# Performance work log

Measured on AMD Instinct MI355X. Metric: run time of the kernel, lower is better.

Reference implementation:

```python
import jax, jax.numpy as jnp
import numpy as np

IN_F = 256
LAYERS = [256, 256, 256, 256]   # layer_sizeList
DIMS = [IN_F] + LAYERS          # per-layer (in, out) = (DIMS[i], DIMS[i+1])
NUM_L = len(LAYERS)             # 4 dynamic layers (3 hidden + final identity)
CASE_IN = 64
CASE_H = 256
W_SIZE = IN_F * LAYERS[0]       # 65536, uniform across layers here
C, N = 64, 2048


def setup_inputs() -> dict:
    key = jax.random.key(0)
    k = jax.random.split(key, 8)
    x = jax.random.normal(k[0], (N, IN_F), jnp.float32)
    o = jax.random.normal(k[1], (C, CASE_IN), jnp.float32)
    # caseNN hidden layer (Linear + SiLU)
    Wc = jax.random.normal(k[2], (CASE_IN, CASE_H), jnp.float32) / np.sqrt(CASE_IN).astype(np.float32)
    bc = jnp.zeros((CASE_H,), jnp.float32)
    # final heads (identity activation): one weight head + one bias head per domain layer
    head_scale = np.float32(1.0 / (np.sqrt(CASE_H) * np.sqrt(IN_F)))
    Ww = jax.random.normal(k[3], (NUM_L, CASE_H, W_SIZE), jnp.float32) * head_scale
    bw = jnp.zeros((NUM_L, W_SIZE), jnp.float32)
    Wb = jax.random.normal(k[4], (NUM_L, CASE_H, LAYERS[0]), jnp.float32) * head_scale
    bb = jnp.zeros((NUM_L, LAYERS[0]), jnp.float32)
    return {"x": x, "o": o, "Wc": Wc, "bc": bc, "Ww": Ww, "bw": bw, "Wb": Wb, "bb": bb}


def reference(x, o, Wc, bc, Ww, bw, Wb, bb):
    # ---- caseNN (hypernetwork): generate per-case weights/biases ----
    h = jax.nn.silu(o @ Wc + bc)                     # [C, H]
    w = jnp.einsum('ch,lhd->lcd', h, Ww) + bw[:, None, :]   # [L, C, in*out]
    b = jnp.einsum('ch,lhd->lcd', h, Wb) + bb[:, None, :]   # [L, C, out]
    c = o.shape[0]

    # ---- domain net: per-case dynamic FC layers with skip connections ----
    # layer 0: broadcast shared x over cases
    W0 = w[0].reshape(c, DIMS[0], DIMS[1])
    y = jax.nn.silu(jnp.einsum('ni,cio->cno', x, W0) + b[0][:, None, :])  # [C, N, 256]
    x_skip = y  # skip_connections and i==0
    for i in range(1, NUM_L - 1):
        Wi = w[i].reshape(c, DIMS[i], DIMS[i + 1])
        y2 = jax.nn.silu(jnp.einsum('cni,cio->cno', y, Wi) + b[i][:, None, :])
        if i % 2 == 0:
            y2, x_skip = y2 + x_skip, y2
        y = y2
    # final layer: identity activation
    Wf = w[NUM_L - 1].reshape(c, DIMS[NUM_L - 1], DIMS[NUM_L])
    out = jnp.einsum('cni,cio->cno', y, Wf) + b[NUM_L - 1][:, None, :]
    return out.reshape(-1, out.shape[-1])  # [C*N, out]
```

## Files before the change

### kernel.cpp

```cpp
#include <hip/hip_runtime.h>


typedef __bf16 bf16;
typedef __bf16 bf16x4 __attribute__((ext_vector_type(4)));
typedef __bf16 bf16x8 __attribute__((ext_vector_type(8)));
typedef float  f32x2  __attribute__((ext_vector_type(2)));
typedef float  f32x4  __attribute__((ext_vector_type(4)));
typedef unsigned short u16x8 __attribute__((ext_vector_type(8)));

#define AS1 __attribute__((address_space(1)))
#define AS3 __attribute__((address_space(3)))

__device__ __forceinline__ void gl2lds16(const void* g, void* l) {
  __builtin_amdgcn_global_load_lds((const AS1 unsigned int*)g,
                                   (AS3 unsigned int*)l, 16, 0, 0);
}

__device__ __forceinline__ float silu_f(float v) {
  return v / (1.0f + __expf(-v));
}

__global__ void k_hyper(const float* __restrict__ o, const float* __restrict__ Wc,
                        const float* __restrict__ bc, float* __restrict__ ht) {
  __shared__ float os[64];
  int c = blockIdx.x;
  int j = threadIdx.x;
  if (j < 64) os[j] = o[c * 64 + j];
  __syncthreads();
  float a = bc[j];
#pragma unroll
  for (int i = 0; i < 64; ++i) a = fmaf(os[i], Wc[i * 256 + j], a);
  ht[j * 64 + c] = silu_f(a);
}

__global__ void k_xcast(const float* __restrict__ x, bf16* __restrict__ xb) {
  int i = (blockIdx.x * 256 + threadIdx.x) * 4;
  float4 v = *(const float4*)(x + i);
  bf16x4 r = { (bf16)v.x, (bf16)v.y, (bf16)v.z, (bf16)v.w };
  *(bf16x4*)(xb + i) = r;
}

__global__ __launch_bounds__(256, 4) void k_genw(const float* __restrict__ Ww,
                                                 const float* __restrict__ bw,
                                                 const float* __restrict__ ht,
                                                 bf16* __restrict__ wnat) {
  int l = blockIdx.x >> 8;
  int d = (blockIdx.x & 255) * 256 + threadIdx.x;
  const float* wp = Ww + (size_t)l * 256 * 65536 + d;
  f32x2 acc[32];
#pragma unroll
  for (int c = 0; c < 32; ++c) acc[c] = (f32x2){0.f, 0.f};
  float wcur = wp[0];
  for (int hh = 0; hh < 256; ++hh) {
    float wnext = (hh < 255) ? wp[(size_t)(hh + 1) * 65536] : 0.f;
    const f32x2* hp = (const f32x2*)(ht + hh * 64);
    f32x2 wv = {wcur, wcur};
#pragma unroll
    for (int c = 0; c < 32; ++c) {
      f32x2 h2 = hp[c];
      acc[c].x = fmaf(h2.x, wv.x, acc[c].x);
      acc[c].y = fmaf(h2.y, wv.y, acc[c].y);
    }
    wcur = wnext;
  }
  float bv = bw[(size_t)l * 65536 + d];
#pragma unroll
  for (int c = 0; c < 32; ++c) {
    wnat[(size_t)(l * 64 + 2 * c) * 65536 + d]     = (bf16)(acc[c].x + bv);
    wnat[(size_t)(l * 64 + 2 * c + 1) * 65536 + d] = (bf16)(acc[c].y + bv);
  }
}

__global__ void k_genb(const float* __restrict__ Wb, const float* __restrict__ bb,
                       const float* __restrict__ ht, float* __restrict__ bias) {
  int l = blockIdx.x >> 6;
  int c = blockIdx.x & 63;
  int oo = threadIdx.x;
  const float* wp = Wb + (size_t)l * 65536 + oo;
  float acc = 0.f;
  for (int hh = 0; hh < 256; ++hh)
    acc = fmaf(ht[hh * 64 + c], wp[hh * 256], acc);
  bias[(size_t)(l * 64 + c) * 256 + oo] = acc + bb[l * 256 + oo];
}

__global__ void k_tw(const unsigned short* __restrict__ w,
                     unsigned short* __restrict__ wt) {
  __shared__ unsigned short T[64][64];
  int b = blockIdx.x;
  int lc = b >> 4, tile = b & 15;
  int i0 = (tile >> 2) << 6, o0 = (tile & 3) << 6;
  const unsigned short* src = w + (size_t)lc * 65536;
  unsigned short* dst = wt + (size_t)lc * 65536;
  int t = threadIdx.x;
  for (int q = t; q < 512; q += 256) {
    int r = q >> 3, cc = q & 7;
    u16x8 v = *(const u16x8*)(src + (size_t)(i0 + r) * 256 + o0 + cc * 8);
    *(u16x8*)&T[r][(cc ^ ((r >> 3) & 7)) * 8] = v;
  }
  __syncthreads();
  for (int q = t; q < 512; q += 256) {
    int r = q >> 3, cc = q & 7;
    u16x8 v;
#pragma unroll
    for (int e = 0; e < 8; ++e) {
      int il = cc * 8 + e;
      v[e] = T[il][((((r >> 3) ^ (il >> 3)) & 7) << 3) + (r & 7)];
    }
    *(u16x8*)(dst + (size_t)(o0 + r) * 256 + i0 + cc * 8) = v;
  }
}

template <int LAYER>
__global__ __launch_bounds__(256, 3) void k_gemm(
    const bf16* __restrict__ A_base, const bf16* __restrict__ WT,
    const float* __restrict__ BIAS, bf16* __restrict__ Yout,
    const bf16* __restrict__ Skip, float* __restrict__ Fout) {
  __shared__ bf16 As[128 * 32];
  __shared__ bf16 Bs[128 * 32];
  int bx = blockIdx.x;
  bx = (bx & 7) * 256 + (bx >> 3);
  int c  = bx >> 5;
  int tl = bx & 31;
  int m0 = (tl & 15) << 7;
  int n0 = (tl >> 4) << 7;
  int tid = threadIdx.x;
  int lane = tid & 63, wid = tid >> 6;
  int wm = wid >> 1, wn = wid & 1;

  const bf16* Ab = (LAYER == 0) ? A_base : (A_base + (size_t)c * 2048 * 256);
  const bf16* Bb = WT + (size_t)c * 65536;

  f32x4 acc[4][4] = {};

  int qb = (wid << 7) + lane;
  int q2 = qb + 64;
  char* lA0 = (char*)As + (wid << 11);
  char* lB0 = (char*)Bs + (wid << 11);

  for (int kk = 0; kk < 8; ++kk) {
    int k0 = kk * 32;
    gl2lds16((const char*)(Ab + (size_t)(m0 + (qb >> 2)) * 256 + k0) + (qb & 3) * 16, lA0);
    gl2lds16((const char*)(Ab + (size_t)(m0 + (q2 >> 2)) * 256 + k0) + (q2 & 3) * 16, lA0 + 1024);
    gl2lds16((const char*)(Bb + (size_t)(n0 + (qb >> 2)) * 256 + k0) + (qb & 3) * 16, lB0);
    gl2lds16((const char*)(Bb + (size_t)(n0 + (q2 >> 2)) * 256 + k0) + (q2 & 3) * 16, lB0 + 1024);
    __syncthreads();

    bf16x8 af[4], bfr[4];
    int krow = (lane >> 4) * 8;
#pragma unroll
    for (int i = 0; i < 4; ++i) {
      af[i]  = *(const bf16x8*)&As[(wm * 64 + i * 16 + (lane & 15)) * 32 + krow];
      bfr[i] = *(const bf16x8*)&Bs[(wn * 64 + i * 16 + (lane & 15)) * 32 + krow];
    }
#pragma unroll
    for (int i = 0; i < 4; ++i)
#pragma unroll
      for (int j = 0; j < 4; ++j)
        acc[i][j] = __builtin_amdgcn_mfma_f32_16x16x32_bf16(af[i], bfr[j],
                                                            acc[i][j], 0, 0, 0);
    __syncthreads();
  }

  const float* bp = BIAS + c * 256;
#pragma unroll
  for (int i = 0; i < 4; ++i) {
    int row = m0 + wm * 64 + i * 16 + (lane >> 4) * 4;
#pragma unroll
    for (int j = 0; j < 4; ++j) {
      int col = n0 + wn * 64 + j * 16 + (lane & 15);
      float bv = bp[col];
#pragma unroll
      for (int r = 0; r < 4; ++r) {
        float v = acc[i][j][r] + bv;
        size_t idx = ((size_t)c * 2048 + (row + r)) * 256 + col;
        if (LAYER < 3) {
          float s = silu_f(v);
          if (LAYER == 2) s += (float)Skip[idx];
          Yout[idx] = (bf16)s;
        } else {
          Fout[idx] = v;
        }
      }
    }
  }
}

extern "C" void kernel_launch(void* const* d_in, const int* in_sizes, int n_in,
                              void* d_out, int out_size, void* d_ws, size_t ws_size,
                              hipStream_t stream) {
  const float* x  = (const float*)d_in[0];
  const float* o  = (const float*)d_in[1];
  const float* Wc = (const float*)d_in[2];
  const float* bc = (const float*)d_in[3];
  const float* Ww = (const float*)d_in[4];
  const float* bw = (const float*)d_in[5];
  const float* Wb = (const float*)d_in[6];
  const float* bb = (const float*)d_in[7];
  float* out = (float*)d_out;
  char* ws = (char*)d_ws;

  if (ws_size < 102039552ULL) return;
  bf16*  wt   = (bf16*)(ws);
  bf16*  buf0 = (bf16*)(ws + 33554432);
  float* bias = (float*)(ws + 100663296);
  float* ht   = (float*)(ws + 100925440);
  bf16*  xb   = (bf16*)(ws + 100990976);
  bf16*  buf1 = (bf16*)(out);
  bf16*  wnat = (bf16*)((char*)out + 67108864);

  k_hyper<<<64, 256, 0, stream>>>(o, Wc, bc, ht);
  k_xcast<<<512, 256, 0, stream>>>(x, xb);
  k_genw<<<1024, 256, 0, stream>>>(Ww, bw, ht, wnat);
  k_genb<<<256, 256, 0, stream>>>(Wb, bb, ht, bias);
  k_tw<<<4096, 256, 0, stream>>>((const unsigned short*)wnat, (unsigned short*)wt);

  k_gemm<0><<<2048, 256, 0, stream>>>(xb,   wt,               bias,             buf0, nullptr, nullptr);
  k_gemm<1><<<2048, 256, 0, stream>>>(buf0, wt + 1 * 4194304, bias + 1 * 16384, buf1, nullptr, nullptr);
  k_gemm<2><<<2048, 256, 0, stream>>>(buf1, wt + 2 * 4194304, bias + 2 * 16384, buf0, buf0,    nullptr);
  k_gemm<3><<<2048, 256, 0, stream>>>(buf0, wt + 3 * 4194304, bias + 3 * 16384, nullptr, nullptr, out);
}
```

Baseline: 686.5 us.

## Move weight generation to fp16 MFMA and triple-buffer GEMM loads

The hypernetwork weight-generation kernel is rewritten from scalar FP32 FMAs into an fp16 MFMA GEMM. The hidden activations are stored in swizzled LDS, and Ww tiles are streamed through a 3-slot LDS ring. The per-layer GEMM kernel gets the same 3-stage global-to-LDS pipeline with explicit vmcnt waits. The bias-generation kernel splits its reduction across 4 thread groups. This cuts the compute-bound generation cost and hides load latency, but it rounds h and Ww to fp16 and uses more LDS per block, which may lower occupancy.

```diff
diff --git a/kernel.cpp b/kernel.cpp
--- a/kernel.cpp
+++ b/kernel.cpp
@@ -4,7 +4,8 @@
 typedef __bf16 bf16;
 typedef __bf16 bf16x4 __attribute__((ext_vector_type(4)));
 typedef __bf16 bf16x8 __attribute__((ext_vector_type(8)));
-typedef float  f32x2  __attribute__((ext_vector_type(2)));
+typedef _Float16 f16;
+typedef _Float16 f16x8 __attribute__((ext_vector_type(8)));
 typedef float  f32x4  __attribute__((ext_vector_type(4)));
 typedef unsigned short u16x8 __attribute__((ext_vector_type(8)));
 
@@ -21,7 +22,8 @@
 }
 
 __global__ void k_hyper(const float* __restrict__ o, const float* __restrict__ Wc,
-                        const float* __restrict__ bc, float* __restrict__ ht) {
+                        const float* __restrict__ bc, float* __restrict__ ht,
+                        f16* __restrict__ hb16) {
   __shared__ float os[64];
   int c = blockIdx.x;
   int j = threadIdx.x;
@@ -30,7 +32,9 @@
   float a = bc[j];
 #pragma unroll
   for (int i = 0; i < 64; ++i) a = fmaf(os[i], Wc[i * 256 + j], a);
-  ht[j * 64 + c] = silu_f(a);
+  float h = silu_f(a);
+  ht[j * 64 + c] = h;
+  hb16[c * 256 + j] = (f16)h;
 }
 
 __global__ void k_xcast(const float* __restrict__ x, bf16* __restrict__ xb) {
@@ -40,52 +44,107 @@
   *(bf16x4*)(xb + i) = r;
 }
 
-__global__ __launch_bounds__(256, 4) void k_genw(const float* __restrict__ Ww,
-                                                 const float* __restrict__ bw,
-                                                 const float* __restrict__ ht,
-                                                 bf16* __restrict__ wnat) {
+__global__ __launch_bounds__(512, 1) void k_genw(
+    const float* __restrict__ Ww, const float* __restrict__ bw,
+    const f16* __restrict__ hb16, bf16* __restrict__ wnat) {
+  __shared__ __attribute__((aligned(16))) char Hs[32768];
+  __shared__ __attribute__((aligned(16))) char Wslot[3][32768];
   int l = blockIdx.x >> 8;
-  int d = (blockIdx.x & 255) * 256 + threadIdx.x;
-  const float* wp = Ww + (size_t)l * 256 * 65536 + d;
-  f32x2 acc[32];
-#pragma unroll
-  for (int c = 0; c < 32; ++c) acc[c] = (f32x2){0.f, 0.f};
-  float wcur = wp[0];
-  for (int hh = 0; hh < 256; ++hh) {
-    float wnext = (hh < 255) ? wp[(size_t)(hh + 1) * 65536] : 0.f;
-    const f32x2* hp = (const f32x2*)(ht + hh * 64);
-    f32x2 wv = {wcur, wcur};
-#pragma unroll
-    for (int c = 0; c < 32; ++c) {
-      f32x2 h2 = hp[c];
-      acc[c].x = fmaf(h2.x, wv.x, acc[c].x);
-      acc[c].y = fmaf(h2.y, wv.y, acc[c].y);
-    }
-    wcur = wnext;
-  }
-  float bv = bw[(size_t)l * 65536 + d];
-#pragma unroll
-  for (int c = 0; c < 32; ++c) {
-    wnat[(size_t)(l * 64 + 2 * c) * 65536 + d]     = (bf16)(acc[c].x + bv);
-    wnat[(size_t)(l * 64 + 2 * c + 1) * 65536 + d] = (bf16)(acc[c].y + bv);
+  int d0 = (blockIdx.x & 255) * 256;
+  const float* Wwl = Ww + (size_t)l * 16777216;
+  int tid = threadIdx.x, lane = tid & 63, wid = tid >> 6;
+
+  for (int q = tid; q < 2048; q += 512) {
+    int c = q >> 5, g = q & 31;
+    f16x8 v = *(const f16x8*)(hb16 + c * 256 + g * 8);
+    *(f16x8*)(Hs + c * 512 + ((g ^ (c & 7)) << 4)) = v;
+  }
+  __syncthreads();
+
+  auto STAGE = [&](int s, int t) {
+#pragma unroll
+    for (int ii = 0; ii < 4; ++ii) {
+      int row = wid * 4 + ii;
+      gl2lds16(Wwl + (size_t)(t * 32 + row) * 65536 + d0 + lane * 4,
+               &Wslot[s][row * 1024]);
+    }
+  };
+
+  f32x4 acc[4][2] = {};
+  STAGE(0, 0);
+  STAGE(1, 1);
+#pragma unroll
+  for (int kk = 0; kk < 8; ++kk) {
+    if (kk < 6) STAGE((kk + 2) % 3, kk + 2);
+    if (kk < 6)       asm volatile("s_waitcnt vmcnt(8)" ::: "memory");
+    else if (kk == 6) asm volatile("s_waitcnt vmcnt(4)" ::: "memory");
+    else              asm volatile("s_waitcnt vmcnt(0)" ::: "memory");
+    __builtin_amdgcn_s_barrier();
+    __builtin_amdgcn_sched_barrier(0);
+
+    f16x8 af[4];
+    int kc = kk * 4 + (lane >> 4);
+#pragma unroll
+    for (int mf = 0; mf < 4; ++mf) {
+      int c = mf * 16 + (lane & 15);
+      af[mf] = *(const f16x8*)(Hs + c * 512 + ((kc ^ (c & 7)) << 4));
+    }
+    const float* Ws = (const float*)&Wslot[kk % 3][0];
+    f16x8 bfrag[2];
+#pragma unroll
+    for (int nf = 0; nf < 2; ++nf) {
+      int n = wid * 32 + nf * 16 + (lane & 15);
+#pragma unroll
+      for (int j = 0; j < 8; ++j)
+        bfrag[nf][j] = (f16)Ws[((lane >> 4) * 8 + j) * 256 + n];
+    }
+    asm volatile("s_waitcnt lgkmcnt(0)" ::: "memory");
+    __builtin_amdgcn_sched_barrier(0);
+    __builtin_amdgcn_s_barrier();
+#pragma unroll
+    for (int mf = 0; mf < 4; ++mf)
+#pragma unroll
+      for (int nf = 0; nf < 2; ++nf)
+        acc[mf][nf] = __builtin_amdgcn_mfma_f32_16x16x32_f16(
+            af[mf], bfrag[nf], acc[mf][nf], 0, 0, 0);
+  }
+
+#pragma unroll
+  for (int nf = 0; nf < 2; ++nf) {
+    int d = d0 + wid * 32 + nf * 16 + (lane & 15);
+    float bv = bw[(size_t)l * 65536 + d];
+#pragma unroll
+    for (int mf = 0; mf < 4; ++mf) {
+      int cb = mf * 16 + (lane >> 4) * 4;
+#pragma unroll
+      for (int r = 0; r < 4; ++r)
+        wnat[(size_t)(l * 64 + cb + r) * 65536 + d] = (bf16)(acc[mf][nf][r] + bv);
+    }
   }
 }
 
 __global__ void k_genb(const float* __restrict__ Wb, const float* __restrict__ bb,
                        const float* __restrict__ ht, float* __restrict__ bias) {
+  __shared__ float red[4][256];
   int l = blockIdx.x >> 6;
   int c = blockIdx.x & 63;
-  int oo = threadIdx.x;
+  int q = threadIdx.x >> 8;
+  int oo = threadIdx.x & 255;
   const float* wp = Wb + (size_t)l * 65536 + oo;
-  float acc = 0.f;
-  for (int hh = 0; hh < 256; ++hh)
-    acc = fmaf(ht[hh * 64 + c], wp[hh * 256], acc);
-  bias[(size_t)(l * 64 + c) * 256 + oo] = acc + bb[l * 256 + oo];
+  float a = 0.f;
+#pragma unroll 4
+  for (int hh = q * 64; hh < q * 64 + 64; ++hh)
+    a = fmaf(ht[hh * 64 + c], wp[hh * 256], a);
+  red[q][oo] = a;
+  __syncthreads();
+  if (q == 0)
+    bias[(size_t)(l * 64 + c) * 256 + oo] =
+        red[0][oo] + red[1][oo] + red[2][oo] + red[3][oo] + bb[l * 256 + oo];
 }
 
 __global__ void k_tw(const unsigned short* __restrict__ w,
                      unsigned short* __restrict__ wt) {
-  __shared__ unsigned short T[64][64];
+  __shared__ __attribute__((aligned(16))) unsigned short T[64][64];
   int b = blockIdx.x;
   int lc = b >> 4, tile = b & 15;
   int i0 = (tile >> 2) << 6, o0 = (tile & 3) << 6;
@@ -115,8 +174,8 @@
     const bf16* __restrict__ A_base, const bf16* __restrict__ WT,
     const float* __restrict__ BIAS, bf16* __restrict__ Yout,
     const bf16* __restrict__ Skip, float* __restrict__ Fout) {
-  __shared__ bf16 As[128 * 32];
-  __shared__ bf16 Bs[128 * 32];
+  __shared__ __attribute__((aligned(16))) bf16 As[3][128 * 32];
+  __shared__ __attribute__((aligned(16))) bf16 Bs[3][128 * 32];
   int bx = blockIdx.x;
   bx = (bx & 7) * 256 + (bx >> 3);
   int c  = bx >> 5;
@@ -130,35 +189,49 @@
   const bf16* Ab = (LAYER == 0) ? A_base : (A_base + (size_t)c * 2048 * 256);
   const bf16* Bb = WT + (size_t)c * 65536;
 
-  f32x4 acc[4][4] = {};
-
   int qb = (wid << 7) + lane;
   int q2 = qb + 64;
-  char* lA0 = (char*)As + (wid << 11);
-  char* lB0 = (char*)Bs + (wid << 11);
-
+
+  auto STAGE = [&](int slot, int t) {
+    int k0 = t * 32;
+    char* lA = (char*)&As[slot][0] + (wid << 11);
+    char* lB = (char*)&Bs[slot][0] + (wid << 11);
+    gl2lds16((const char*)(Ab + (size_t)(m0 + (qb >> 2)) * 256 + k0) + (qb & 3) * 16, lA);
+    gl2lds16((const char*)(Ab + (size_t)(m0 + (q2 >> 2)) * 256 + k0) + (q2 & 3) * 16, lA + 1024);
+    gl2lds16((const char*)(Bb + (size_t)(n0 + (qb >> 2)) * 256 + k0) + (qb & 3) * 16, lB);
+    gl2lds16((const char*)(Bb + (size_t)(n0 + (q2 >> 2)) * 256 + k0) + (q2 & 3) * 16, lB + 1024);
+  };
+
+  f32x4 acc[4][4] = {};
+  STAGE(0, 0);
+  STAGE(1, 1);
+#pragma unroll
   for (int kk = 0; kk < 8; ++kk) {
-    int k0 = kk * 32;
-    gl2lds16((const char*)(Ab + (size_t)(m0 + (qb >> 2)) * 256 + k0) + (qb & 3) * 16, lA0);
-    gl2lds16((const char*)(Ab + (size_t)(m0 + (q2 >> 2)) * 256 + k0) + (q2 & 3) * 16, lA0 + 1024);
-    gl2lds16((const char*)(Bb + (size_t)(n0 + (qb >> 2)) * 256 + k0) + (qb & 3) * 16, lB0);
-    gl2lds16((const char*)(Bb + (size_t)(n0 + (q2 >> 2)) * 256 + k0) + (q2 & 3) * 16, lB0 + 1024);
-    __syncthreads();
-
+    if (kk < 6) STAGE((kk + 2) % 3, kk + 2);
+    if (kk < 6)       asm volatile("s_waitcnt vmcnt(8)" ::: "memory");
+    else if (kk == 6) asm volatile("s_waitcnt vmcnt(4)" ::: "memory");
+    else              asm volatile("s_waitcnt vmcnt(0)" ::: "memory");
+    __builtin_amdgcn_s_barrier();
+    __builtin_amdgcn_sched_barrier(0);
+
+    const bf16* Asl = &As[kk % 3][0];
+    const bf16* Bsl = &Bs[kk % 3][0];
     bf16x8 af[4], bfr[4];
     int krow = (lane >> 4) * 8;
 #pragma unroll
     for (int i = 0; i < 4; ++i) {
-      af[i]  = *(const bf16x8*)&As[(wm * 64 + i * 16 + (lane & 15)) * 32 + krow];
-      bfr[i] = *(const bf16x8*)&Bs[(wn * 64 + i * 16 + (lane & 15)) * 32 + krow];
-    }
+      af[i]  = *(const bf16x8*)&Asl[(wm * 64 + i * 16 + (lane & 15)) * 32 + krow];
+      bfr[i] = *(const bf16x8*)&Bsl[(wn * 64 + i * 16 + (lane & 15)) * 32 + krow];
+    }
+    asm volatile("s_waitcnt lgkmcnt(0)" ::: "memory");
+    __builtin_amdgcn_sched_barrier(0);
+    __builtin_amdgcn_s_barrier();
 #pragma unroll
     for (int i = 0; i < 4; ++i)
 #pragma unroll
       for (int j = 0; j < 4; ++j)
         acc[i][j] = __builtin_amdgcn_mfma_f32_16x16x32_bf16(af[i], bfr[j],
                                                             acc[i][j], 0, 0, 0);
-    __syncthreads();
   }
 
   const float* bp = BIAS + c * 256;
@@ -199,19 +272,20 @@
   float* out = (float*)d_out;
   char* ws = (char*)d_ws;
 
-  if (ws_size < 102039552ULL) return;
+  if (ws_size < 102072320ULL) return;
   bf16*  wt   = (bf16*)(ws);
   bf16*  buf0 = (bf16*)(ws + 33554432);
   float* bias = (float*)(ws + 100663296);
   float* ht   = (float*)(ws + 100925440);
   bf16*  xb   = (bf16*)(ws + 100990976);
+  f16*   hb16 = (f16*)(ws + 102039552);
   bf16*  buf1 = (bf16*)(out);
   bf16*  wnat = (bf16*)((char*)out + 67108864);
 
-  k_hyper<<<64, 256, 0, stream>>>(o, Wc, bc, ht);
+  k_hyper<<<64, 256, 0, stream>>>(o, Wc, bc, ht, hb16);
   k_xcast<<<512, 256, 0, stream>>>(x, xb);
-  k_genw<<<1024, 256, 0, stream>>>(Ww, bw, ht, wnat);
-  k_genb<<<256, 256, 0, stream>>>(Wb, bb, ht, bias);
+  k_genw<<<1024, 512, 0, stream>>>(Ww, bw, hb16, wnat);
+  k_genb<<<256, 1024, 0, stream>>>(Wb, bb, ht, bias);
   k_tw<<<4096, 256, 0, stream>>>((const unsigned short*)wnat, (unsigned short*)wt);
 
   k_gemm<0><<<2048, 256, 0, stream>>>(xb,   wt,               bias,             buf0, nullptr, nullptr);
```

After: 579.7 us. 15.6% less time.
